# Performance work log

Measured on AMD Instinct MI355X. Metric: run time of the kernel, lower is better.

Reference implementation:

```python
import jax, jax.numpy as jnp
import numpy as np

B, L, D = 4, 2048, 256
PH, EH = 64, 256
MAX_DISP = 5.0
MIN_DISP = 0.5
REP = 0.3
POWER = 2.0
SURFACE = 103.0
NROW = 46
OFFSET = 0.1
SPACING = SURFACE / (NROW - 1)
DANGER = SPACING / 4.0


def _gelu(x):
    return jax.nn.gelu(x, approximate=False)  # torch nn.GELU default = exact erf


def setup_inputs() -> dict:
    key = jax.random.key(0)
    ks = jax.random.split(key, 8)

    def lin(k, i, o):
        return jax.random.normal(k, (i, o), jnp.float32) * 0.02, jnp.zeros((o,), jnp.float32)

    pe_w1, pe_b1 = lin(ks[0], 2, PH)
    pe_w2, pe_b2 = lin(ks[1], PH, PH)
    em_w1, em_b1 = lin(ks[2], D + PH, EH)
    em_w2, em_b2 = lin(ks[3], EH, EH // 2)
    em_w3, em_b3 = lin(ks[4], EH // 2, 1)
    ln_g = jnp.ones((EH,), jnp.float32)
    ln_b = jnp.zeros((EH,), jnp.float32)
    latents = jax.random.normal(ks[5], (B, L, D), jnp.float32)
    positions = jax.random.uniform(ks[6], (B, L, 2), jnp.float32) * SURFACE
    return dict(latents=latents, positions=positions,
                pe_w1=pe_w1, pe_b1=pe_b1, pe_w2=pe_w2, pe_b2=pe_b2,
                em_w1=em_w1, em_b1=em_b1, ln_g=ln_g, ln_b=ln_b,
                em_w2=em_w2, em_b2=em_b2, em_w3=em_w3, em_b3=em_b3,
                layer_idx=0)


def _predict_errors(latents, positions, pe_w1, pe_b1, pe_w2, pe_b2,
                    em_w1, em_b1, ln_g, ln_b, em_w2, em_b2, em_w3, em_b3):
    # ErrorPredictor: pos encoder MLP + error MLP with LayerNorm + Softplus
    pf = _gelu(positions @ pe_w1 + pe_b1) @ pe_w2 + pe_b2          # [B,L,PH]
    x = jnp.concatenate([latents, pf], axis=-1)                     # [B,L,D+PH]
    h = x @ em_w1 + em_b1                                           # [B,L,EH]
    mu = h.mean(-1, keepdims=True)
    var = ((h - mu) ** 2).mean(-1, keepdims=True)
    h = (h - mu) / jnp.sqrt(var + 1e-5) * ln_g + ln_b
    h = _gelu(h)
    h = _gelu(h @ em_w2 + em_b2)                                    # [B,L,EH//2]
    return jax.nn.softplus(h @ em_w3 + em_b3)[..., 0]               # [B,L]


def _forward(latents, positions, pe_w1, pe_b1, pe_w2, pe_b2,
             em_w1, em_b1, ln_g, ln_b, em_w2, em_b2, em_w3, em_b3):
    # error prediction on detached inputs
    errors = _predict_errors(jax.lax.stop_gradient(latents), jax.lax.stop_gradient(positions),
                             pe_w1, pe_b1, pe_w2, pe_b2,
                             em_w1, em_b1, ln_g, ln_b, em_w2, em_b2, em_w3, em_b3)
    e_min = errors.min(-1, keepdims=True)
    e_max = errors.max(-1, keepdims=True)
    errors_norm = (errors - e_min) / (e_max - e_min + 1e-8) + OFFSET  # [B,L]

    # all-pairs delta_ij = pos_j - pos_i : [B,L,L,2]
    delta = positions[:, None, :, :] - positions[:, :, None, :]
    dist = jnp.maximum(jnp.sqrt((delta ** 2).sum(-1)), 1e-6)          # [B,L,L]
    direction = delta / dist[..., None]
    mask = ~jnp.eye(L, dtype=bool)                                    # exclude self

    gmag = (errors_norm[:, None, :] / dist ** POWER) * mask           # [B,L,L]
    gravity = (direction * gmag[..., None]).sum(axis=2)               # [B,L,2]

    viol = jnp.maximum(DANGER - dist, 0.0)
    rmag = (jnp.exp(viol / DANGER) - 1.0) * mask
    repulsion = -(direction * rmag[..., None]).sum(axis=2)            # [B,L,2]

    total = gravity + REP * repulsion
    fmag = jnp.sqrt((total ** 2).sum(-1, keepdims=True))              # [B,L,1]
    fdir = total / (fmag + 1e-8)
    fmean = fmag.mean(axis=1, keepdims=True)
    frel = fmag / (fmean + 1e-8)
    dmag = jnp.clip(frel * MAX_DISP, MIN_DISP, MAX_DISP)
    displacement = fdir * dmag
    new_positions = positions + displacement
    return new_positions, displacement, errors


def reference(latents, positions, pe_w1, pe_b1, pe_w2, pe_b2,
              em_w1, em_b1, ln_g, ln_b, em_w2, em_b2, em_w3, em_b3, layer_idx):
    # share_weights=True -> layer_idx selects the same predictor
    return _forward(latents, positions, pe_w1, pe_b1, pe_w2, pe_b2,
                    em_w1, em_b1, ln_g, ln_b, em_w2, em_b2, em_w3, em_b3)
```

## Files before the change

### kernel.cpp

```cpp
#include <hip/hip_runtime.h>
#include <math.h>

#define NB 4
#define NL 2048
#define ND 256
#define PPB 16

__device__ __forceinline__ float gelu_exact(float x) {
    return 0.5f * x * (1.0f + erff(x * 0.70710678118654752f));
}

#define DANGER_F ((float)(103.0 / 45.0 / 4.0))
#define DANGER2_SLACK_F ((float)(103.0 / 45.0 / 4.0 * 103.0 / 45.0 / 4.0 * 1.0001))
#define REP_F 0.3f
#define MAXD_F 5.0f
#define MIND_F 0.5f
#define OFF_F 0.1f

__global__ __launch_bounds__(512) void mlp_kernel(
    const float* __restrict__ latents, const float* __restrict__ positions,
    const float* __restrict__ pe_w1, const float* __restrict__ pe_b1,
    const float* __restrict__ pe_w2, const float* __restrict__ pe_b2,
    const float* __restrict__ em_w1, const float* __restrict__ em_b1,
    const float* __restrict__ ln_g, const float* __restrict__ ln_b,
    const float* __restrict__ em_w2, const float* __restrict__ em_b2,
    const float* __restrict__ em_w3, const float* __restrict__ em_b3,
    float* __restrict__ errors_out)
{
    const int t  = threadIdx.x;
    const int g0 = blockIdx.x * PPB;
    const int l  = t & 63;
    const int p0 = (t >> 6) * 2;

    __shared__ float xs[PPB][320];
    __shared__ float pf1[PPB][64];
    __shared__ float posl[2 * PPB];

    {
        const float4* src = (const float4*)(latents + (size_t)g0 * ND);
        #pragma unroll
        for (int m = 0; m < 2; ++m) {
            const int q = t + 512 * m;
            const float4 v = src[q];
            *(float4*)&xs[q >> 6][(q & 63) * 4] = v;
        }
    }
    if (t < PPB) ((float2*)posl)[t] = ((const float2*)positions)[g0 + t];
    __syncthreads();

    {
        const int p = t >> 5, j0 = t & 31;
        const float px = posl[2 * p], py = posl[2 * p + 1];
        #pragma unroll
        for (int h = 0; h < 2; ++h) {
            const int j = j0 + 32 * h;
            pf1[p][j] = gelu_exact(fmaf(px, pe_w1[j], fmaf(py, pe_w1[64 + j], pe_b1[j])));
        }
    }
    __syncthreads();
    {
        const int p = t >> 5, j0 = t & 31;
        #pragma unroll
        for (int h = 0; h < 2; ++h) {
            const int j = j0 + 32 * h;
            float a = pe_b2[j];
            #pragma unroll 4
            for (int k = 0; k < 64; ++k)
                a = fmaf(pf1[p][k], pe_w2[k * 64 + j], a);
            xs[p][ND + j] = a;
        }
    }
    __syncthreads();

    float4 acc0 = *(const float4*)&em_b1[4 * l];
    float4 acc1 = acc0;
    {
        const float4* __restrict__ W1 = (const float4*)em_w1;
        #pragma unroll 2
        for (int k = 0; k < 320; k += 4) {
            const float4 xq0 = *(const float4*)&xs[p0][k];
            const float4 xq1 = *(const float4*)&xs[p0 + 1][k];
            const float xa0[4] = {xq0.x, xq0.y, xq0.z, xq0.w};
            const float xa1[4] = {xq1.x, xq1.y, xq1.z, xq1.w};
            #pragma unroll
            for (int u = 0; u < 4; ++u) {
                const float4 w = W1[(size_t)(k + u) * 64 + l];
                acc0.x = fmaf(xa0[u], w.x, acc0.x);
                acc0.y = fmaf(xa0[u], w.y, acc0.y);
                acc0.z = fmaf(xa0[u], w.z, acc0.z);
                acc0.w = fmaf(xa0[u], w.w, acc0.w);
                acc1.x = fmaf(xa1[u], w.x, acc1.x);
                acc1.y = fmaf(xa1[u], w.y, acc1.y);
                acc1.z = fmaf(xa1[u], w.z, acc1.z);
                acc1.w = fmaf(xa1[u], w.w, acc1.w);
            }
        }
    }

    float s0 = acc0.x + acc0.y + acc0.z + acc0.w;
    float q0 = acc0.x * acc0.x + acc0.y * acc0.y + acc0.z * acc0.z + acc0.w * acc0.w;
    float s1 = acc1.x + acc1.y + acc1.z + acc1.w;
    float q1 = acc1.x * acc1.x + acc1.y * acc1.y + acc1.z * acc1.z + acc1.w * acc1.w;
    #pragma unroll
    for (int m = 1; m < 64; m <<= 1) {
        s0 += __shfl_xor(s0, m); q0 += __shfl_xor(q0, m);
        s1 += __shfl_xor(s1, m); q1 += __shfl_xor(q1, m);
    }
    const float mu0 = s0 * (1.0f / 256.0f);
    const float rs0 = 1.0f / sqrtf(q0 * (1.0f / 256.0f) - mu0 * mu0 + 1e-5f);
    const float mu1 = s1 * (1.0f / 256.0f);
    const float rs1 = 1.0f / sqrtf(q1 * (1.0f / 256.0f) - mu1 * mu1 + 1e-5f);

    {
        const float4 g4 = *(const float4*)&ln_g[4 * l];
        const float4 b4 = *(const float4*)&ln_b[4 * l];
        float4 o0, o1;
        o0.x = gelu_exact(fmaf((acc0.x - mu0) * rs0, g4.x, b4.x));
        o0.y = gelu_exact(fmaf((acc0.y - mu0) * rs0, g4.y, b4.y));
        o0.z = gelu_exact(fmaf((acc0.z - mu0) * rs0, g4.z, b4.z));
        o0.w = gelu_exact(fmaf((acc0.w - mu0) * rs0, g4.w, b4.w));
        o1.x = gelu_exact(fmaf((acc1.x - mu1) * rs1, g4.x, b4.x));
        o1.y = gelu_exact(fmaf((acc1.y - mu1) * rs1, g4.y, b4.y));
        o1.z = gelu_exact(fmaf((acc1.z - mu1) * rs1, g4.z, b4.z));
        o1.w = gelu_exact(fmaf((acc1.w - mu1) * rs1, g4.w, b4.w));
        *(float4*)&xs[p0][4 * l]     = o0;
        *(float4*)&xs[p0 + 1][4 * l] = o1;
    }

    float2 a0 = *(const float2*)&em_b2[2 * l];
    float2 a1 = a0;
    {
        const float2* __restrict__ W2 = (const float2*)em_w2;
        #pragma unroll 2
        for (int k = 0; k < 256; k += 4) {
            const float4 xq0 = *(const float4*)&xs[p0][k];
            const float4 xq1 = *(const float4*)&xs[p0 + 1][k];
            const float xa0[4] = {xq0.x, xq0.y, xq0.z, xq0.w};
            const float xa1[4] = {xq1.x, xq1.y, xq1.z, xq1.w};
            #pragma unroll
            for (int u = 0; u < 4; ++u) {
                const float2 w = W2[(size_t)(k + u) * 64 + l];
                a0.x = fmaf(xa0[u], w.x, a0.x);
                a0.y = fmaf(xa0[u], w.y, a0.y);
                a1.x = fmaf(xa1[u], w.x, a1.x);
                a1.y = fmaf(xa1[u], w.y, a1.y);
            }
        }
    }

    {
        const float2 w3 = *(const float2*)&em_w3[2 * l];
        float rA = fmaf(gelu_exact(a0.x), w3.x, gelu_exact(a0.y) * w3.y);
        float rB = fmaf(gelu_exact(a1.x), w3.x, gelu_exact(a1.y) * w3.y);
        #pragma unroll
        for (int m = 1; m < 64; m <<= 1) {
            rA += __shfl_xor(rA, m);
            rB += __shfl_xor(rB, m);
        }
        if (l == 0) {
            const float xA = rA + em_b3[0];
            const float xB = rB + em_b3[0];
            errors_out[g0 + p0]     = fmaxf(xA, 0.0f) + log1pf(expf(-fabsf(xA)));
            errors_out[g0 + p0 + 1] = fmaxf(xB, 0.0f) + log1pf(expf(-fabsf(xB)));
        }
    }
}

__global__ __launch_bounds__(256) void norm_kernel(const float* __restrict__ errors,
                                                   float* __restrict__ errn)
{
    const int b = blockIdx.x, t = threadIdx.x;
    const float* e = errors + b * NL;
    float v[8], mn = 1e30f, mx = -1e30f;
    #pragma unroll
    for (int m = 0; m < 8; ++m) {
        v[m] = e[t + 256 * m];
        mn = fminf(mn, v[m]); mx = fmaxf(mx, v[m]);
    }
    #pragma unroll
    for (int m = 1; m < 64; m <<= 1) {
        mn = fminf(mn, __shfl_xor(mn, m));
        mx = fmaxf(mx, __shfl_xor(mx, m));
    }
    __shared__ float rmn[4], rmx[4];
    const int lane = t & 63, wid = t >> 6;
    if (lane == 0) { rmn[wid] = mn; rmx[wid] = mx; }
    __syncthreads();
    mn = fminf(fminf(rmn[0], rmn[1]), fminf(rmn[2], rmn[3]));
    mx = fmaxf(fmaxf(rmx[0], rmx[1]), fmaxf(rmx[2], rmx[3]));
    const float den = mx - mn + 1e-8f;
    #pragma unroll
    for (int m = 0; m < 8; ++m)
        errn[b * NL + t + 256 * m] = (v[m] - mn) / den + OFF_F;
}

template <int S>
__global__ __launch_bounds__(256) void pair_kernel(
    const float* __restrict__ positions, const float* __restrict__ errn,
    float2* __restrict__ partials)
{
    constexpr int JC = NL / S;
    const int t = threadIdx.x;
    int bid = blockIdx.x;
    const int jc = bid % S; bid /= S;
    const int ic = bid & 7;
    const int b  = bid >> 3;
    const int i  = ic * 256 + t;

    const float2 pi = ((const float2*)positions)[b * NL + i];

    __shared__ float4 pj4[JC];
    const int j0 = jc * JC;
    for (int m = t; m < JC; m += 256) {
        const float2 pj = ((const float2*)positions)[b * NL + j0 + m];
        pj4[m] = make_float4(pj.x, pj.y, errn[b * NL + j0 + m], 0.0f);
    }
    __syncthreads();

    float tx = 0.f, ty = 0.f;
    #pragma unroll 4
    for (int m = 0; m < JC; ++m) {
        const float4 v = pj4[m];
        const float dx = v.x - pi.x;
        const float dy = v.y - pi.y;
        const float r2 = fmaf(dx, dx, dy * dy);
        const bool tiny = (r2 < 1e-12f);
        const float invd = tiny ? 1e6f : rsqrtf(r2);
        float w = v.z * invd * invd;
        if (r2 < DANGER2_SLACK_F) {
            const float dist = fmaxf(sqrtf(r2), 1e-6f);
            const float viol = DANGER_F - dist;
            if (viol > 0.f)
                w -= REP_F * (expf(viol / DANGER_F) - 1.0f);
        }
        const float g = w * invd;
        tx = fmaf(dx, g, tx);
        ty = fmaf(dy, g, ty);
    }
    partials[((size_t)jc * NB + b) * NL + i] = make_float2(tx, ty);
}

template <int S>
__global__ __launch_bounds__(512) void final_kernel(
    const float* __restrict__ positions, const float2* __restrict__ partials,
    float* __restrict__ out)
{
    const int b = blockIdx.x, t = threadIdx.x;
    float tx[4], ty[4], fm[4];
    float fsum = 0.f;
    #pragma unroll
    for (int m = 0; m < 4; ++m) {
        const int i = t + 512 * m;
        float sx = 0.f, sy = 0.f;
        #pragma unroll
        for (int s = 0; s < S; ++s) {
            const float2 v = partials[((size_t)s * NB + b) * NL + i];
            sx += v.x; sy += v.y;
        }
        tx[m] = sx; ty[m] = sy;
        fm[m] = sqrtf(fmaf(sx, sx, sy * sy));
        fsum += fm[m];
    }
    #pragma unroll
    for (int m = 1; m < 64; m <<= 1) fsum += __shfl_xor(fsum, m);
    __shared__ float rs[8];
    const int lane = t & 63, wid = t >> 6;
    if (lane == 0) rs[wid] = fsum;
    __syncthreads();
    float fmean = 0.f;
    #pragma unroll
    for (int w = 0; w < 8; ++w) fmean += rs[w];
    fmean *= (1.0f / NL);

    float* newpos = out;
    float* disp   = out + 2 * NB * NL;
    #pragma unroll
    for (int m = 0; m < 4; ++m) {
        const int i = t + 512 * m;
        const float fmag = fm[m];
        const float frel = fmag / (fmean + 1e-8f);
        const float dmag = fminf(fmaxf(frel * MAXD_F, MIND_F), MAXD_F);
        const float fdx = tx[m] / (fmag + 1e-8f);
        const float fdy = ty[m] / (fmag + 1e-8f);
        const float dpx = fdx * dmag, dpy = fdy * dmag;
        const float2 pi = ((const float2*)positions)[b * NL + i];
        ((float2*)newpos)[b * NL + i] = make_float2(pi.x + dpx, pi.y + dpy);
        ((float2*)disp)[b * NL + i]   = make_float2(dpx, dpy);
    }
}

extern "C" void kernel_launch(void* const* d_in, const int* in_sizes, int n_in,
                              void* d_out, int out_size, void* d_ws, size_t ws_size,
                              hipStream_t stream)
{
    const float* latents   = (const float*)d_in[0];
    const float* positions = (const float*)d_in[1];
    const float* pe_w1 = (const float*)d_in[2];
    const float* pe_b1 = (const float*)d_in[3];
    const float* pe_w2 = (const float*)d_in[4];
    const float* pe_b2 = (const float*)d_in[5];
    const float* em_w1 = (const float*)d_in[6];
    const float* em_b1 = (const float*)d_in[7];
    const float* ln_g  = (const float*)d_in[8];
    const float* ln_b  = (const float*)d_in[9];
    const float* em_w2 = (const float*)d_in[10];
    const float* em_b2 = (const float*)d_in[11];
    const float* em_w3 = (const float*)d_in[12];
    const float* em_b3 = (const float*)d_in[13];

    float* out = (float*)d_out;
    float* errors = out + 2 * 2 * NB * NL;

    float* ws = (float*)d_ws;
    float* errn = ws;
    float2* partials = (float2*)(ws + NB * NL);

    int S = 32;
    const size_t avail = ws_size / sizeof(float);
    while (S > 1 && (size_t)NB * NL + (size_t)S * NB * 2 * NL > avail) S >>= 1;

    mlp_kernel<<<NB * NL / PPB, 512, 0, stream>>>(
        latents, positions, pe_w1, pe_b1, pe_w2, pe_b2,
        em_w1, em_b1, ln_g, ln_b, em_w2, em_b2, em_w3, em_b3, errors);

    norm_kernel<<<NB, 256, 0, stream>>>(errors, errn);

    const int grid = NB * (NL / 256) * S;
    switch (S) {
        case 32: pair_kernel<32><<<grid, 256, 0, stream>>>(positions, errn, partials); break;
        case 16: pair_kernel<16><<<grid, 256, 0, stream>>>(positions, errn, partials); break;
        case 8:  pair_kernel<8> <<<grid, 256, 0, stream>>>(positions, errn, partials); break;
        case 4:  pair_kernel<4> <<<grid, 256, 0, stream>>>(positions, errn, partials); break;
        case 2:  pair_kernel<2> <<<grid, 256, 0, stream>>>(positions, errn, partials); break;
        default: pair_kernel<1> <<<grid, 256, 0, stream>>>(positions, errn, partials); break;
    }

    switch (S) {
        case 32: final_kernel<32><<<NB, 512, 0, stream>>>(positions, partials, out); break;
        case 16: final_kernel<16><<<NB, 512, 0, stream>>>(positions, partials, out); break;
        case 8:  final_kernel<8> <<<NB, 512, 0, stream>>>(positions, partials, out); break;
        case 4:  final_kernel<4> <<<NB, 512, 0, stream>>>(positions, partials, out); break;
        case 2:  final_kernel<2> <<<NB, 512, 0, stream>>>(positions, partials, out); break;
        default: final_kernel<1> <<<NB, 512, 0, stream>>>(positions, partials, out); break;
    }
}
```

Baseline: 193.8 us.

## Raise MLP register tiling, prefetch weights, and use atomic force accumulation

The MLP kernel now handles 32 points per block with 4 points per wave. Each weight load is reused across four rows, and weight chunks are double-buffered in registers to hide global load latency. The pair stage drops the per-split partial buffer and template selection. It normalizes errors on the fly from a per-batch min/denominator pair, fixes S=32 with 64 j per block, and accumulates forces with atomicAdd into a buffer zeroed by the min/max kernel. This trades partial-sum traffic and the final reduction loop for atomics and nondeterministic summation order, and it doubles MLP register pressure.

```diff
diff --git a/kernel.cpp b/kernel.cpp
--- a/kernel.cpp
+++ b/kernel.cpp
@@ -4,7 +4,7 @@
 #define NB 4
 #define NL 2048
 #define ND 256
-#define PPB 16
+#define PPB 32
 
 __device__ __forceinline__ float gelu_exact(float x) {
     return 0.5f * x * (1.0f + erff(x * 0.70710678118654752f));
@@ -30,7 +30,7 @@
     const int t  = threadIdx.x;
     const int g0 = blockIdx.x * PPB;
     const int l  = t & 63;
-    const int p0 = (t >> 6) * 2;
+    const int p0 = (t >> 6) * 4;
 
     __shared__ float xs[PPB][320];
     __shared__ float pf1[PPB][64];
@@ -39,7 +39,7 @@
     {
         const float4* src = (const float4*)(latents + (size_t)g0 * ND);
         #pragma unroll
-        for (int m = 0; m < 2; ++m) {
+        for (int m = 0; m < 4; ++m) {
             const int q = t + 512 * m;
             const float4 v = src[q];
             *(float4*)&xs[q >> 6][(q & 63) * 4] = v;
@@ -49,20 +49,20 @@
     __syncthreads();
 
     {
-        const int p = t >> 5, j0 = t & 31;
+        const int p = t >> 4, j0 = t & 15;
         const float px = posl[2 * p], py = posl[2 * p + 1];
         #pragma unroll
-        for (int h = 0; h < 2; ++h) {
-            const int j = j0 + 32 * h;
+        for (int h = 0; h < 4; ++h) {
+            const int j = j0 + 16 * h;
             pf1[p][j] = gelu_exact(fmaf(px, pe_w1[j], fmaf(py, pe_w1[64 + j], pe_b1[j])));
         }
     }
     __syncthreads();
     {
-        const int p = t >> 5, j0 = t & 31;
-        #pragma unroll
-        for (int h = 0; h < 2; ++h) {
-            const int j = j0 + 32 * h;
+        const int p = t >> 4, j0 = t & 15;
+        #pragma unroll
+        for (int h = 0; h < 4; ++h) {
+            const int j = j0 + 16 * h;
             float a = pe_b2[j];
             #pragma unroll 4
             for (int k = 0; k < 64; ++k)
@@ -72,110 +72,161 @@
     }
     __syncthreads();
 
-    float4 acc0 = *(const float4*)&em_b1[4 * l];
-    float4 acc1 = acc0;
+    float acc[4][4];
+    {
+        const float4 b1 = *(const float4*)&em_b1[4 * l];
+        #pragma unroll
+        for (int p = 0; p < 4; ++p) {
+            acc[p][0] = b1.x; acc[p][1] = b1.y; acc[p][2] = b1.z; acc[p][3] = b1.w;
+        }
+    }
+
+#define MM_CHUNK(KK, W)                                                          \
+    {                                                                            \
+        float xk[4][4];                                                          \
+        _Pragma("unroll")                                                        \
+        for (int p = 0; p < 4; ++p) {                                            \
+            const float4 xq = *(const float4*)&xs[p0 + p][(KK)];                 \
+            xk[p][0] = xq.x; xk[p][1] = xq.y; xk[p][2] = xq.z; xk[p][3] = xq.w;  \
+        }                                                                        \
+        _Pragma("unroll")                                                        \
+        for (int u = 0; u < 4; ++u) {                                            \
+            _Pragma("unroll")                                                    \
+            for (int p = 0; p < 4; ++p) {                                        \
+                acc[p][0] = fmaf(xk[p][u], W[u].x, acc[p][0]);                   \
+                acc[p][1] = fmaf(xk[p][u], W[u].y, acc[p][1]);                   \
+                acc[p][2] = fmaf(xk[p][u], W[u].z, acc[p][2]);                   \
+                acc[p][3] = fmaf(xk[p][u], W[u].w, acc[p][3]);                   \
+            }                                                                    \
+        }                                                                        \
+    }
+
     {
         const float4* __restrict__ W1 = (const float4*)em_w1;
-        #pragma unroll 2
-        for (int k = 0; k < 320; k += 4) {
-            const float4 xq0 = *(const float4*)&xs[p0][k];
-            const float4 xq1 = *(const float4*)&xs[p0 + 1][k];
-            const float xa0[4] = {xq0.x, xq0.y, xq0.z, xq0.w};
-            const float xa1[4] = {xq1.x, xq1.y, xq1.z, xq1.w};
-            #pragma unroll
-            for (int u = 0; u < 4; ++u) {
-                const float4 w = W1[(size_t)(k + u) * 64 + l];
-                acc0.x = fmaf(xa0[u], w.x, acc0.x);
-                acc0.y = fmaf(xa0[u], w.y, acc0.y);
-                acc0.z = fmaf(xa0[u], w.z, acc0.z);
-                acc0.w = fmaf(xa0[u], w.w, acc0.w);
-                acc1.x = fmaf(xa1[u], w.x, acc1.x);
-                acc1.y = fmaf(xa1[u], w.y, acc1.y);
-                acc1.z = fmaf(xa1[u], w.z, acc1.z);
-                acc1.w = fmaf(xa1[u], w.w, acc1.w);
-            }
-        }
-    }
-
-    float s0 = acc0.x + acc0.y + acc0.z + acc0.w;
-    float q0 = acc0.x * acc0.x + acc0.y * acc0.y + acc0.z * acc0.z + acc0.w * acc0.w;
-    float s1 = acc1.x + acc1.y + acc1.z + acc1.w;
-    float q1 = acc1.x * acc1.x + acc1.y * acc1.y + acc1.z * acc1.z + acc1.w * acc1.w;
-    #pragma unroll
-    for (int m = 1; m < 64; m <<= 1) {
-        s0 += __shfl_xor(s0, m); q0 += __shfl_xor(q0, m);
-        s1 += __shfl_xor(s1, m); q1 += __shfl_xor(q1, m);
-    }
-    const float mu0 = s0 * (1.0f / 256.0f);
-    const float rs0 = 1.0f / sqrtf(q0 * (1.0f / 256.0f) - mu0 * mu0 + 1e-5f);
-    const float mu1 = s1 * (1.0f / 256.0f);
-    const float rs1 = 1.0f / sqrtf(q1 * (1.0f / 256.0f) - mu1 * mu1 + 1e-5f);
+        float4 wA[4], wB[4];
+        #pragma unroll
+        for (int u = 0; u < 4; ++u) wA[u] = W1[(size_t)(0 + u) * 64 + l];
+        #pragma unroll
+        for (int u = 0; u < 4; ++u) wB[u] = W1[(size_t)(4 + u) * 64 + l];
+        for (int k = 0; k < 312; k += 8) {
+            MM_CHUNK(k, wA);
+            #pragma unroll
+            for (int u = 0; u < 4; ++u) wA[u] = W1[(size_t)(k + 8 + u) * 64 + l];
+            MM_CHUNK(k + 4, wB);
+            #pragma unroll
+            for (int u = 0; u < 4; ++u) wB[u] = W1[(size_t)(k + 12 + u) * 64 + l];
+        }
+        MM_CHUNK(312, wA);
+        MM_CHUNK(316, wB);
+    }
+#undef MM_CHUNK
+
+    float mu[4], rstd[4];
+    #pragma unroll
+    for (int p = 0; p < 4; ++p) {
+        float s = acc[p][0] + acc[p][1] + acc[p][2] + acc[p][3];
+        float q = acc[p][0] * acc[p][0] + acc[p][1] * acc[p][1]
+                + acc[p][2] * acc[p][2] + acc[p][3] * acc[p][3];
+        #pragma unroll
+        for (int m = 1; m < 64; m <<= 1) {
+            s += __shfl_xor(s, m);
+            q += __shfl_xor(q, m);
+        }
+        mu[p] = s * (1.0f / 256.0f);
+        rstd[p] = 1.0f / sqrtf(q * (1.0f / 256.0f) - mu[p] * mu[p] + 1e-5f);
+    }
 
     {
         const float4 g4 = *(const float4*)&ln_g[4 * l];
         const float4 b4 = *(const float4*)&ln_b[4 * l];
-        float4 o0, o1;
-        o0.x = gelu_exact(fmaf((acc0.x - mu0) * rs0, g4.x, b4.x));
-        o0.y = gelu_exact(fmaf((acc0.y - mu0) * rs0, g4.y, b4.y));
-        o0.z = gelu_exact(fmaf((acc0.z - mu0) * rs0, g4.z, b4.z));
-        o0.w = gelu_exact(fmaf((acc0.w - mu0) * rs0, g4.w, b4.w));
-        o1.x = gelu_exact(fmaf((acc1.x - mu1) * rs1, g4.x, b4.x));
-        o1.y = gelu_exact(fmaf((acc1.y - mu1) * rs1, g4.y, b4.y));
-        o1.z = gelu_exact(fmaf((acc1.z - mu1) * rs1, g4.z, b4.z));
-        o1.w = gelu_exact(fmaf((acc1.w - mu1) * rs1, g4.w, b4.w));
-        *(float4*)&xs[p0][4 * l]     = o0;
-        *(float4*)&xs[p0 + 1][4 * l] = o1;
-    }
-
-    float2 a0 = *(const float2*)&em_b2[2 * l];
-    float2 a1 = a0;
+        #pragma unroll
+        for (int p = 0; p < 4; ++p) {
+            float4 o;
+            o.x = gelu_exact(fmaf((acc[p][0] - mu[p]) * rstd[p], g4.x, b4.x));
+            o.y = gelu_exact(fmaf((acc[p][1] - mu[p]) * rstd[p], g4.y, b4.y));
+            o.z = gelu_exact(fmaf((acc[p][2] - mu[p]) * rstd[p], g4.z, b4.z));
+            o.w = gelu_exact(fmaf((acc[p][3] - mu[p]) * rstd[p], g4.w, b4.w));
+            *(float4*)&xs[p0 + p][4 * l] = o;
+        }
+    }
+
+    float a2[4][2];
+    {
+        const float2 b2 = *(const float2*)&em_b2[2 * l];
+        #pragma unroll
+        for (int p = 0; p < 4; ++p) { a2[p][0] = b2.x; a2[p][1] = b2.y; }
+    }
+
+#define H2_CHUNK(KK, W)                                                          \
+    {                                                                            \
+        float xk[4][4];                                                          \
+        _Pragma("unroll")                                                        \
+        for (int p = 0; p < 4; ++p) {                                            \
+            const float4 xq = *(const float4*)&xs[p0 + p][(KK)];                 \
+            xk[p][0] = xq.x; xk[p][1] = xq.y; xk[p][2] = xq.z; xk[p][3] = xq.w;  \
+        }                                                                        \
+        _Pragma("unroll")                                                        \
+        for (int u = 0; u < 4; ++u) {                                            \
+            _Pragma("unroll")                                                    \
+            for (int p = 0; p < 4; ++p) {                                        \
+                a2[p][0] = fmaf(xk[p][u], W[u].x, a2[p][0]);                     \
+                a2[p][1] = fmaf(xk[p][u], W[u].y, a2[p][1]);                     \
+            }                                                                    \
+        }                                                                        \
+    }
+
     {
         const float2* __restrict__ W2 = (const float2*)em_w2;
-        #pragma unroll 2
-        for (int k = 0; k < 256; k += 4) {
-            const float4 xq0 = *(const float4*)&xs[p0][k];
-            const float4 xq1 = *(const float4*)&xs[p0 + 1][k];
-            const float xa0[4] = {xq0.x, xq0.y, xq0.z, xq0.w};
-            const float xa1[4] = {xq1.x, xq1.y, xq1.z, xq1.w};
-            #pragma unroll
-            for (int u = 0; u < 4; ++u) {
-                const float2 w = W2[(size_t)(k + u) * 64 + l];
-                a0.x = fmaf(xa0[u], w.x, a0.x);
-                a0.y = fmaf(xa0[u], w.y, a0.y);
-                a1.x = fmaf(xa1[u], w.x, a1.x);
-                a1.y = fmaf(xa1[u], w.y, a1.y);
+        float2 wA[4], wB[4];
+        #pragma unroll
+        for (int u = 0; u < 4; ++u) wA[u] = W2[(size_t)(0 + u) * 64 + l];
+        #pragma unroll
+        for (int u = 0; u < 4; ++u) wB[u] = W2[(size_t)(4 + u) * 64 + l];
+        for (int k = 0; k < 248; k += 8) {
+            H2_CHUNK(k, wA);
+            #pragma unroll
+            for (int u = 0; u < 4; ++u) wA[u] = W2[(size_t)(k + 8 + u) * 64 + l];
+            H2_CHUNK(k + 4, wB);
+            #pragma unroll
+            for (int u = 0; u < 4; ++u) wB[u] = W2[(size_t)(k + 12 + u) * 64 + l];
+        }
+        H2_CHUNK(248, wA);
+        H2_CHUNK(252, wB);
+    }
+#undef H2_CHUNK
+
+    {
+        const float2 w3 = *(const float2*)&em_w3[2 * l];
+        float r[4];
+        #pragma unroll
+        for (int p = 0; p < 4; ++p)
+            r[p] = fmaf(gelu_exact(a2[p][0]), w3.x, gelu_exact(a2[p][1]) * w3.y);
+        #pragma unroll
+        for (int m = 1; m < 64; m <<= 1) {
+            #pragma unroll
+            for (int p = 0; p < 4; ++p) r[p] += __shfl_xor(r[p], m);
+        }
+        if (l == 0) {
+            #pragma unroll
+            for (int p = 0; p < 4; ++p) {
+                const float x = r[p] + em_b3[0];
+                errors_out[g0 + p0 + p] = fmaxf(x, 0.0f) + log1pf(expf(-fabsf(x)));
             }
         }
     }
-
-    {
-        const float2 w3 = *(const float2*)&em_w3[2 * l];
-        float rA = fmaf(gelu_exact(a0.x), w3.x, gelu_exact(a0.y) * w3.y);
-        float rB = fmaf(gelu_exact(a1.x), w3.x, gelu_exact(a1.y) * w3.y);
-        #pragma unroll
-        for (int m = 1; m < 64; m <<= 1) {
-            rA += __shfl_xor(rA, m);
-            rB += __shfl_xor(rB, m);
-        }
-        if (l == 0) {
-            const float xA = rA + em_b3[0];
-            const float xB = rB + em_b3[0];
-            errors_out[g0 + p0]     = fmaxf(xA, 0.0f) + log1pf(expf(-fabsf(xA)));
-            errors_out[g0 + p0 + 1] = fmaxf(xB, 0.0f) + log1pf(expf(-fabsf(xB)));
-        }
-    }
-}
-
-__global__ __launch_bounds__(256) void norm_kernel(const float* __restrict__ errors,
-                                                   float* __restrict__ errn)
+}
+
+__global__ __launch_bounds__(256) void minmax_kernel(const float* __restrict__ errors,
+                                                     float2* __restrict__ mnden,
+                                                     float2* __restrict__ force)
 {
     const int b = blockIdx.x, t = threadIdx.x;
     const float* e = errors + b * NL;
-    float v[8], mn = 1e30f, mx = -1e30f;
+    float mn = 1e30f, mx = -1e30f;
     #pragma unroll
     for (int m = 0; m < 8; ++m) {
-        v[m] = e[t + 256 * m];
-        mn = fminf(mn, v[m]); mx = fmaxf(mx, v[m]);
+        const float v = e[t + 256 * m];
+        mn = fminf(mn, v); mx = fmaxf(mx, v);
     }
     #pragma unroll
     for (int m = 1; m < 64; m <<= 1) {
@@ -186,40 +237,41 @@
     const int lane = t & 63, wid = t >> 6;
     if (lane == 0) { rmn[wid] = mn; rmx[wid] = mx; }
     __syncthreads();
-    mn = fminf(fminf(rmn[0], rmn[1]), fminf(rmn[2], rmn[3]));
-    mx = fmaxf(fmaxf(rmx[0], rmx[1]), fmaxf(rmx[2], rmx[3]));
-    const float den = mx - mn + 1e-8f;
+    if (t == 0) {
+        mn = fminf(fminf(rmn[0], rmn[1]), fminf(rmn[2], rmn[3]));
+        mx = fmaxf(fmaxf(rmx[0], rmx[1]), fmaxf(rmx[2], rmx[3]));
+        mnden[b] = make_float2(mn, (mx - mn) + 1e-8f);
+    }
     #pragma unroll
     for (int m = 0; m < 8; ++m)
-        errn[b * NL + t + 256 * m] = (v[m] - mn) / den + OFF_F;
-}
-
-template <int S>
+        force[b * NL + t + 256 * m] = make_float2(0.0f, 0.0f);
+}
+
 __global__ __launch_bounds__(256) void pair_kernel(
-    const float* __restrict__ positions, const float* __restrict__ errn,
-    float2* __restrict__ partials)
-{
-    constexpr int JC = NL / S;
+    const float* __restrict__ positions, const float* __restrict__ errors,
+    const float2* __restrict__ mnden, float2* __restrict__ force)
+{
     const int t = threadIdx.x;
     int bid = blockIdx.x;
-    const int jc = bid % S; bid /= S;
-    const int ic = bid & 7;
-    const int b  = bid >> 3;
+    const int jc = bid & 31; bid >>= 5;
+    const int ic = bid & 7;  bid >>= 3;
+    const int b  = bid;
     const int i  = ic * 256 + t;
 
     const float2 pi = ((const float2*)positions)[b * NL + i];
 
-    __shared__ float4 pj4[JC];
-    const int j0 = jc * JC;
-    for (int m = t; m < JC; m += 256) {
-        const float2 pj = ((const float2*)positions)[b * NL + j0 + m];
-        pj4[m] = make_float4(pj.x, pj.y, errn[b * NL + j0 + m], 0.0f);
+    __shared__ float4 pj4[64];
+    if (t < 64) {
+        const int j = jc * 64 + t;
+        const float2 pj = ((const float2*)positions)[b * NL + j];
+        const float2 md = mnden[b];
+        pj4[t] = make_float4(pj.x, pj.y, (errors[b * NL + j] - md.x) / md.y + OFF_F, 0.0f);
     }
     __syncthreads();
 
     float tx = 0.f, ty = 0.f;
     #pragma unroll 4
-    for (int m = 0; m < JC; ++m) {
+    for (int m = 0; m < 64; ++m) {
         const float4 v = pj4[m];
         const float dx = v.x - pi.x;
         const float dy = v.y - pi.y;
@@ -237,12 +289,12 @@
         tx = fmaf(dx, g, tx);
         ty = fmaf(dy, g, ty);
     }
-    partials[((size_t)jc * NB + b) * NL + i] = make_float2(tx, ty);
-}
-
-template <int S>
+    atomicAdd(&force[b * NL + i].x, tx);
+    atomicAdd(&force[b * NL + i].y, ty);
+}
+
 __global__ __launch_bounds__(512) void final_kernel(
-    const float* __restrict__ positions, const float2* __restrict__ partials,
+    const float* __restrict__ positions, const float2* __restrict__ force,
     float* __restrict__ out)
 {
     const int b = blockIdx.x, t = threadIdx.x;
@@ -251,14 +303,9 @@
     #pragma unroll
     for (int m = 0; m < 4; ++m) {
         const int i = t + 512 * m;
-        float sx = 0.f, sy = 0.f;
-        #pragma unroll
-        for (int s = 0; s < S; ++s) {
-            const float2 v = partials[((size_t)s * NB + b) * NL + i];
-            sx += v.x; sy += v.y;
-        }
-        tx[m] = sx; ty[m] = sy;
-        fm[m] = sqrtf(fmaf(sx, sx, sy * sy));
+        const float2 v = force[b * NL + i];
+        tx[m] = v.x; ty[m] = v.y;
+        fm[m] = sqrtf(fmaf(v.x, v.x, v.y * v.y));
         fsum += fm[m];
     }
     #pragma unroll
@@ -311,36 +358,16 @@
     float* out = (float*)d_out;
     float* errors = out + 2 * 2 * NB * NL;
 
-    float* ws = (float*)d_ws;
-    float* errn = ws;
-    float2* partials = (float2*)(ws + NB * NL);
-
-    int S = 32;
-    const size_t avail = ws_size / sizeof(float);
-    while (S > 1 && (size_t)NB * NL + (size_t)S * NB * 2 * NL > avail) S >>= 1;
+    float2* mnden = (float2*)d_ws;
+    float2* force = mnden + NB;
 
     mlp_kernel<<<NB * NL / PPB, 512, 0, stream>>>(
         latents, positions, pe_w1, pe_b1, pe_w2, pe_b2,
         em_w1, em_b1, ln_g, ln_b, em_w2, em_b2, em_w3, em_b3, errors);
 
-    norm_kernel<<<NB, 256, 0, stream>>>(errors, errn);
-
-    const int grid = NB * (NL / 256) * S;
-    switch (S) {
-        case 32: pair_kernel<32><<<grid, 256, 0, stream>>>(positions, errn, partials); break;
-        case 16: pair_kernel<16><<<grid, 256, 0, stream>>>(positions, errn, partials); break;
-        case 8:  pair_kernel<8> <<<grid, 256, 0, stream>>>(positions, errn, partials); break;
-        case 4:  pair_kernel<4> <<<grid, 256, 0, stream>>>(positions, errn, partials); break;
-        case 2:  pair_kernel<2> <<<grid, 256, 0, stream>>>(positions, errn, partials); break;
-        default: pair_kernel<1> <<<grid, 256, 0, stream>>>(positions, errn, partials); break;
-    }
-
-    switch (S) {
-        case 32: final_kernel<32><<<NB, 512, 0, stream>>>(positions, partials, out); break;
-        case 16: final_kernel<16><<<NB, 512, 0, stream>>>(positions, partials, out); break;
-        case 8:  final_kernel<8> <<<NB, 512, 0, stream>>>(positions, partials, out); break;
-        case 4:  final_kernel<4> <<<NB, 512, 0, stream>>>(positions, partials, out); break;
-        case 2:  final_kernel<2> <<<NB, 512, 0, stream>>>(positions, partials, out); break;
-        default: final_kernel<1> <<<NB, 512, 0, stream>>>(positions, partials, out); break;
-    }
-}
+    minmax_kernel<<<NB, 256, 0, stream>>>(errors, mnden, force);
+
+    pair_kernel<<<NB * 8 * 32, 256, 0, stream>>>(positions, errors, mnden, force);
+
+    final_kernel<<<NB, 512, 0, stream>>>(positions, force, out);
+}
```

Result: faster. 163.2 us (-15.8%).
